# Kernel optimization log

Measured on AMD Instinct MI355X. Metric: run time of the kernel, lower is better.

The kernel has to match this reference:

```python
import jax, jax.numpy as jnp
import numpy as np

T, B, E, H = 64, 64, 128, 256
N_ITEMS, N_DATA = 50000, 20000
EPS = 1e-8


def setup_inputs() -> dict:
    key = jax.random.key(0)
    ks = jax.random.split(key, 20)
    lengths = jnp.sort(jax.random.randint(ks[0], (B,), 1, T + 1))[::-1]
    lengths = lengths.at[0].set(T)  # pack_padded_sequence expects max length first
    x = jax.random.randint(ks[1], (T, B), 1, N_ITEMS)
    tmask = jnp.arange(T)[:, None] < lengths[None, :]
    x = jnp.where(tmask, x, 0)  # padding index 0
    s = 0.05
    emb_table = (jax.random.normal(ks[2], (N_ITEMS, E)) * s).at[0].set(0.0)  # padding_idx=0
    data_embeddings = jax.random.normal(ks[3], (N_DATA, E)) * s
    return {
        'x': x, 'lengths': lengths,
        'emb_table': emb_table, 'data_embeddings': data_embeddings,
        'W_ih': jax.random.normal(ks[4], (4 * H, E)) * s,
        'W_hh': jax.random.normal(ks[5], (4 * H, H)) * s,
        'b_ih': jax.random.normal(ks[6], (4 * H,)) * s,
        'b_hh': jax.random.normal(ks[7], (4 * H,)) * s,
        'Wq': jax.random.normal(ks[8], (H, H)) * s, 'bq': jax.random.normal(ks[9], (H,)) * s,
        'Wk': jax.random.normal(ks[10], (H, H)) * s, 'bk': jax.random.normal(ks[11], (H,)) * s,
        'Wv': jax.random.normal(ks[12], (H, H)) * s, 'bv': jax.random.normal(ks[13], (H,)) * s,
        'W_out': jax.random.normal(ks[14], (E, H)) * s, 'b_out': jax.random.normal(ks[15], (E,)) * s,
    }


def _forward(x, lengths, emb_table, data_embeddings, W_ih, W_hh, b_ih, b_hh,
             Wq, bq, Wk, bk, Wv, bv, W_out, b_out):
    t_len, b_sz = x.shape
    e_dim = emb_table.shape[1]
    h_dim = W_hh.shape[1]

    embs0 = emb_table[x]  # (T, B, E); dropout is identity in eval mode
    initial_embs = jax.lax.stop_gradient(embs0)  # .clone().detach() in original

    # PositionalEncoding: original slices by x.size(1) == batch dim (faithful quirk)
    pos = jnp.arange(b_sz, dtype=jnp.float32)[:, None]
    div = jnp.exp(jnp.arange(0, e_dim, 2, dtype=jnp.float32) * (-jnp.log(10000.0) / e_dim))
    enc = jnp.stack([jnp.sin(pos * div), jnp.cos(pos * div)], axis=-1).reshape(b_sz, e_dim)
    embs = embs0 + enc[None, :, :]  # broadcast over time

    # single-layer LSTM over time (gate order i, f, g, o)
    def step(carry, x_t):
        h, c = carry
        gates = x_t @ W_ih.T + h @ W_hh.T + (b_ih + b_hh)  # (B, 4H)
        i, f, g, o = jnp.split(gates, 4, axis=-1)
        c = jax.nn.sigmoid(f) * c + jax.nn.sigmoid(i) * jnp.tanh(g)
        h = jax.nn.sigmoid(o) * jnp.tanh(c)
        return (h, c), h

    h0 = jnp.zeros((b_sz, h_dim), embs.dtype)
    (_, _), lstm_out = jax.lax.scan(step, (h0, h0), embs)  # (T, B, H)

    # pack/pad round-trip zeroes outputs past each length (LSTM is causal)
    tmask = jnp.arange(t_len)[:, None] < lengths[None, :]  # (T, B)
    lstm_out = lstm_out * tmask[:, :, None]
    lstm_out = lstm_out.transpose(1, 0, 2)  # (B, T, H)

    padding_mask = jnp.sum(lstm_out, axis=-1) != 0  # (B, T)

    q = lstm_out @ Wq.T + bq
    k = lstm_out @ Wk.T + bk
    v = lstm_out @ Wv.T + bv
    score = jnp.einsum('bth,bsh->bts', q, k) / jnp.sqrt(jnp.float32(h_dim))
    score = jnp.where(padding_mask[:, None, :], score, -jnp.inf)
    attn = jax.nn.softmax(score, axis=2)
    weighted = jnp.einsum('bts,bsh->bth', attn, v)  # (B, T, H)
    attn_output = jnp.mean(weighted, axis=1) @ W_out.T + b_out  # (B, E)

    # kNN: fused normalize + matmul + argmin + gather over all T at once
    qn = initial_embs / jnp.clip(jnp.linalg.norm(initial_embs, axis=-1, keepdims=True), EPS)
    dn = data_embeddings / jnp.clip(jnp.linalg.norm(data_embeddings, axis=-1, keepdims=True), EPS)
    sims = jnp.einsum('tbe,ne->tbn', qn, dn)  # (T, B, N_DATA)
    idx = jnp.argmax(sims, axis=-1)  # argmin of (1 - sim)
    closest = jnp.mean(data_embeddings[idx], axis=0)  # (B, E)

    attn_output = attn_output * closest
    return attn_output @ emb_table.T  # (B, n_items)


def reference(x, lengths, emb_table, data_embeddings, W_ih, W_hh, b_ih, b_hh,
              Wq, bq, Wk, bk, Wv, bv, W_out, b_out):
    return _forward(x, lengths, emb_table, data_embeddings, W_ih, W_hh, b_ih, b_hh,
                    Wq, bq, Wk, bk, Wv, bv, W_out, b_out)
```

## Files before the change

kernel.cpp:

```cpp
#include <hip/hip_runtime.h>

typedef unsigned int uint;
typedef unsigned short ushort;
typedef unsigned long long u64;

#define NITEMS 50000
#define NDATA  20000
#define BLKCAP 4096u
#define OVCAP  65536u

#define OFF_LSTMOUT   0x0000000ULL
#define OFF_HX        0x0400000ULL
#define OFF_HXM       0x0440000ULL
#define OFF_PACKED    0x0480000ULL
#define OFF_PACKED2   0x0488000ULL
#define OFF_HITCNTS   0x0490000ULL
#define OFF_OHITCNT   0x0490800ULL
#define MEMSET_BYTES  0x0491000ULL
#define OFF_QMARGIN   0x0491000ULL
#define OFF_XW        0x05A0000ULL
#define OFF_QKV       0x15A0000ULL
#define OFF_HITBUF    OFF_QKV
#define OFF_WIHT      0x21A0000ULL
#define OFF_WQKVT     0x2220000ULL
#define OFF_BIASIH    0x22E0000ULL
#define OFF_BQKV      0x22E1000ULL
#define OFF_DNSCALE   0x22E2000ULL
#define OFF_AV        0x22FE000ULL
#define OFF_DEMB16    0x2306000ULL
#define OFF_A16       0x27E8000ULL
#define OFF_OVF       0x28E8000ULL

__device__ __forceinline__ ushort f2bf(float f) {
  union { float f; uint u; } v; v.f = f;
  uint u = v.u;
  return (ushort)((u + 0x7FFFu + ((u >> 16) & 1u)) >> 16);
}
__device__ __forceinline__ uint fkey(float f) {
  union { float f; uint u; } v; v.f = f;
  return (v.u & 0x80000000u) ? ~v.u : (v.u | 0x80000000u);
}
__device__ __forceinline__ u64 shfl_xor_u64(u64 v, int off) {
  uint lo = (uint)v, hi = (uint)(v >> 32);
  lo = (uint)__shfl_xor((int)lo, off);
  hi = (uint)__shfl_xor((int)hi, off);
  return ((u64)hi << 32) | (u64)lo;
}

typedef __attribute__((ext_vector_type(8))) short short8;
typedef __attribute__((ext_vector_type(4))) float floatx4;

#define R32(M) M(0) M(1) M(2) M(3) M(4) M(5) M(6) M(7) M(8) M(9) M(10) M(11) \
  M(12) M(13) M(14) M(15) M(16) M(17) M(18) M(19) M(20) M(21) M(22) M(23) \
  M(24) M(25) M(26) M(27) M(28) M(29) M(30) M(31)

#define HIX(j) ((j) + (((j) >> 7) << 2))

#define LBAR() do { \
  __builtin_amdgcn_sched_barrier(0); \
  asm volatile("s_waitcnt lgkmcnt(0)" ::: "memory"); \
  __builtin_amdgcn_s_barrier(); \
  __builtin_amdgcn_sched_barrier(0); \
} while (0)

__global__ __launch_bounds__(256) void prep_kernel(
    const int* __restrict__ x,
    const float* __restrict__ emb, const float* __restrict__ demb,
    const float* __restrict__ W_ih,
    const float* __restrict__ Wq, const float* __restrict__ Wk, const float* __restrict__ Wv,
    const float* __restrict__ b_ih, const float* __restrict__ b_hh,
    const float* __restrict__ bq, const float* __restrict__ bk, const float* __restrict__ bv,
    float* __restrict__ dnscale, ushort* __restrict__ demb16, ushort* __restrict__ a16,
    float* __restrict__ wiht, float* __restrict__ wqkvt,
    float* __restrict__ biasih, float* __restrict__ bqkv,
    float* __restrict__ qmargin, u64* __restrict__ packed2)
{
  int blk = blockIdx.x, tid = threadIdx.x;
  if (blk < 5000) {
    int row = blk * 4 + (tid >> 6);
    int lane = tid & 63;
    float2 d = *(const float2*)(demb + (size_t)row * 128 + lane * 2);
    float s = d.x * d.x + d.y * d.y;
    for (int off = 32; off; off >>= 1) s += __shfl_xor(s, off);
    if (lane == 0) dnscale[row] = 1.0f / fmaxf(sqrtf(s), 1e-8f);
  } else if (blk < 6250) {
    size_t base = ((size_t)(blk - 5000) * 256 + tid) * 8;
    float4 f1 = *(const float4*)(demb + base);
    float4 f2 = *(const float4*)(demb + base + 4);
    uint4 o;
    o.x = (uint)f2bf(f1.x) | ((uint)f2bf(f1.y) << 16);
    o.y = (uint)f2bf(f1.z) | ((uint)f2bf(f1.w) << 16);
    o.z = (uint)f2bf(f2.x) | ((uint)f2bf(f2.y) << 16);
    o.w = (uint)f2bf(f2.z) | ((uint)f2bf(f2.w) << 16);
    *(uint4*)(demb16 + base) = o;
  } else if (blk < 6506) {
    int idx = (blk - 6250) * 256 + tid;
    int m = idx >> 4, seg = idx & 15;
    const float* src = emb + (size_t)x[m] * 128 + seg * 8;
    float4 f1 = *(const float4*)(src);
    float4 f2 = *(const float4*)(src + 4);
    uint4 o;
    o.x = (uint)f2bf(f1.x) | ((uint)f2bf(f1.y) << 16);
    o.y = (uint)f2bf(f1.z) | ((uint)f2bf(f1.w) << 16);
    o.z = (uint)f2bf(f2.x) | ((uint)f2bf(f2.y) << 16);
    o.w = (uint)f2bf(f2.z) | ((uint)f2bf(f2.w) << 16);
    *(uint4*)(a16 + (size_t)m * 128 + seg * 8) = o;
  } else if (blk < 7018) {
    int f = (blk - 6506) * 256 + tid;
    int r = f >> 7, e = f & 127;
    wiht[e * 1024 + r] = W_ih[f];
  } else if (blk < 7786) {
    int f = (blk - 7018) * 256 + tid;
    int w = f >> 16; int rem = f & 65535;
    int r = rem >> 8, e = rem & 255;
    const float* src = (w == 0) ? Wq : (w == 1) ? Wk : Wv;
    wqkvt[e * 768 + w * 256 + r] = src[rem];
  } else if (blk < 7790) {
    int idx = (blk - 7786) * 256 + tid;
    if (idx < 1024) biasih[idx] = b_ih[idx] + b_hh[idx];
  } else if (blk < 7793) {
    int idx = (blk - 7790) * 256 + tid;
    if (idx < 768) {
      int w = idx >> 8; int r = idx & 255;
      const float* src = (w == 0) ? bq : (w == 1) ? bk : bv;
      bqkv[idx] = src[r];
    }
  } else {
    int row = (blk - 7793) * 4 + (tid >> 6);
    int lane = tid & 63;
    float2 d = *(const float2*)(emb + (size_t)x[row] * 128 + lane * 2);
    float s = d.x * d.x + d.y * d.y;
    for (int off = 32; off; off >>= 1) s += __shfl_xor(s, off);
    if (lane == 0) {
      if (s == 0.f) {
        qmargin[row] = -1e30f;
        packed2[row] = ((u64)fkey(0.0f) << 32) | 0xFFFFFFFFull;
      } else {
        qmargin[row] = 0.017f * sqrtf(s) + 1e-5f;
      }
    }
  }
}

__global__ __launch_bounds__(256) void xw_kernel(
    const int* __restrict__ x, const float* __restrict__ emb,
    const float* __restrict__ wiht, const float* __restrict__ biasih,
    float* __restrict__ xW)
{
  __shared__ __align__(16) float At[128 * 16];
  int blk = blockIdx.x, tid = threadIdx.x;
  int m0 = blk * 16;
  for (int c = 0; c < 8; ++c) {
    int idx = c * 256 + tid;
    int mm = idx >> 7, e = idx & 127;
    int m = m0 + mm;
    int bcol = m & 63;
    int xv = x[m];
    float val = emb[(size_t)xv * 128 + e];
    int j = e >> 1;
    float arg = (float)bcol * __expf((float)j * -0.14391157f);
    val += (e & 1) ? cosf(arg) : sinf(arg);
    At[e * 16 + mm] = val;
  }
  __syncthreads();
  int quad = tid >> 6, l = tid & 63;
  for (int rp = 0; rp < 4; ++rp) {
    int r = rp * 256 + l * 4;
    float acc[4][4] = {};
    for (int e = 0; e < 128; ++e) {
      float4 wv4 = *(const float4*)(wiht + e * 1024 + r);
      float4 av4 = *(const float4*)(At + e * 16 + quad * 4);
      float am[4] = {av4.x, av4.y, av4.z, av4.w};
      float wr4[4] = {wv4.x, wv4.y, wv4.z, wv4.w};
      #pragma unroll
      for (int mi = 0; mi < 4; ++mi)
        #pragma unroll
        for (int ri = 0; ri < 4; ++ri)
          acc[mi][ri] += am[mi] * wr4[ri];
    }
    float4 bv4 = *(const float4*)(biasih + r);
    #pragma unroll
    for (int mi = 0; mi < 4; ++mi) {
      size_t m = (size_t)(m0 + quad * 4 + mi);
      float4 o;
      o.x = acc[mi][0] + bv4.x; o.y = acc[mi][1] + bv4.y;
      o.z = acc[mi][2] + bv4.z; o.w = acc[mi][3] + bv4.w;
      *(float4*)(xW + m * 1024 + r) = o;
    }
  }
}

__global__ __launch_bounds__(512, 2) void lstm_knn_kernel(
    const int* __restrict__ lengths, const float* __restrict__ Whh,
    const float* __restrict__ xW, float* __restrict__ lstm_out,
    u64* __restrict__ hx, u64* __restrict__ hxm,
    const ushort* __restrict__ a16, const ushort* __restrict__ demb16,
    const float* __restrict__ dnscale, const float* __restrict__ qmargin,
    u64* __restrict__ packed, uint* __restrict__ hitcnts, uint* __restrict__ ohitcnt,
    uint* __restrict__ hitbuf, uint* __restrict__ ovbuf,
    const int* __restrict__ x, const float* __restrict__ emb,
    const float* __restrict__ demb, u64* __restrict__ packed2)
{
  __shared__ __align__(16) float h_sh[264];
  __shared__ float part_sh[256];
  __shared__ __align__(16) ushort b_sh[2][64 * 144];
  __shared__ uint lcnt;
  int tid = threadIdx.x;

  if (blockIdx.x < 256) {
    int blk = blockIdx.x;
    int b = blk & 63, q = blk >> 6;
    int row_local = tid >> 1, half = tid & 1;
    int gate = row_local >> 6, jloc = row_local & 63;
    int grow = gate * 256 + q * 64 + jloc;
    const float4* wp4 = (const float4*)(Whh + (size_t)grow * 256 + half * 128);
#define WDECL(i) float4 tt##i = wp4[i]; \
  float w##i##x = tt##i.x, w##i##y = tt##i.y, w##i##z = tt##i.z, w##i##w = tt##i.w;
    R32(WDECL)
#define WPIN(i) asm volatile("" : "+v"(w##i##x), "+v"(w##i##y), "+v"(w##i##z), "+v"(w##i##w));
    R32(WPIN)
    int len = lengths[b];
    if (tid < 256) h_sh[HIX(tid)] = 0.f;
    float cval = 0.f;
    int prm = tid - 320;
    int jr = (prm < q * 64) ? prm : prm + 64;
    bool fast_ok = true;
    int j1 = q * 64 + (tid - 64);
    float xw0 = 0.f, xw1 = 0.f, xw2 = 0.f, xw3 = 0.f;
    if (tid < 64) {
      const float* xwrow = xW + ((size_t)0 * 64 + b) * 1024 + q * 64 + tid;
      xw0 = xwrow[0]; xw1 = xwrow[256]; xw2 = xwrow[512]; xw3 = xwrow[768];
    }
    __syncthreads();
    for (int t = 0; t < len; ++t) {
      float nx0 = 0.f, nx1 = 0.f, nx2 = 0.f, nx3 = 0.f;
      if (tid < 64 && t + 1 < len) {
        const float* xwrow = xW + ((size_t)(t + 1) * 64 + b) * 1024 + q * 64 + tid;
        nx0 = xwrow[0]; nx1 = xwrow[256]; nx2 = xwrow[512]; nx3 = xwrow[768];
      }
      float hprev = 0.f;
      if (tid >= 64 && tid < 128 && t > 0) hprev = h_sh[HIX(j1)];
      const float4* h4 = (const float4*)(h_sh + half * 132);
      float a[4] = {0.f, 0.f, 0.f, 0.f};
#define WACC(i) { float4 hv_ = h4[i]; \
    a[(i) & 3] += w##i##x * hv_.x + w##i##y * hv_.y + w##i##z * hv_.z + w##i##w * hv_.w; }
      R32(WACC)
      float acc = (a[0] + a[2]) + (a[1] + a[3]);
      acc += __shfl_xor(acc, 1);
      if (!half) part_sh[row_local] = acc;
      LBAR();
      if (tid < 64) {
        float gi = part_sh[tid]       + xw0;
        float gf = part_sh[64 + tid]  + xw1;
        float gg = part_sh[128 + tid] + xw2;
        float go = part_sh[192 + tid] + xw3;
        float ii = 1.f / (1.f + __expf(-gi));
        float ff = 1.f / (1.f + __expf(-gf));
        float oo = 1.f / (1.f + __expf(-go));
        float tg = 1.f - 2.f / (1.f + __expf(2.f * gg));
        cval = ff * cval + ii * tg;
        float tc = 1.f - 2.f / (1.f + __expf(2.f * cval));
        float hv = oo * tc;
        int j = q * 64 + tid;
        union { float f; uint u; } cu; cu.f = hv;
        u64 pk = ((u64)cu.u << 32) | (u64)(uint)(t + 1);
        size_t slot = ((size_t)((t + 1) & 1) * 64 + b) * 256 + j;
        __builtin_amdgcn_sched_barrier(0);
        asm volatile("s_waitcnt vmcnt(4)" ::: "memory");
        asm volatile("global_store_dwordx2 %0, %1, off"
                     :: "v"(hxm + slot), "v"(pk) : "memory");
        __hip_atomic_store(hx + slot, pk, __ATOMIC_RELAXED, __HIP_MEMORY_SCOPE_AGENT);
        h_sh[HIX(j)] = hv;
        xw0 = nx0; xw1 = nx1; xw2 = nx2; xw3 = nx3;
      } else if (tid < 128) {
        if (t > 0) lstm_out[((size_t)b * 64 + (t - 1)) * 256 + j1] = hprev;
      } else if (tid >= 320 && t + 1 < len) {
        size_t slot = ((size_t)((t + 1) & 1) * 64 + b) * 256 + jr;
        uint want = (uint)(t + 1);
        u64 v = 0;
        bool got = false;
        if (fast_ok) {
          const u64* ms = hxm + slot;
          for (int tries = 0; tries < 32; ++tries) {
            asm volatile("global_load_dwordx2 %0, %1, off sc0\n\t"
                         "s_waitcnt vmcnt(0)"
                         : "=&v"(v) : "v"(ms) : "memory");
            if ((uint)v == want) { got = true; break; }
          }
          if (!got && t > 0) fast_ok = false;
        }
        if (!got) {
          const u64* as = hx + slot;
          int guard = 0;
          while (true) {
            v = __hip_atomic_load(as, __ATOMIC_RELAXED, __HIP_MEMORY_SCOPE_AGENT);
            if ((uint)v == want || ++guard > (1 << 24)) break;
          }
        }
        union { uint u; float f; } cv; cv.u = (uint)(v >> 32);
        h_sh[HIX(jr)] = cv.f;
      }
      LBAR();
    }
    if (tid >= 64 && tid < 128) {
      float hl = h_sh[HIX(j1)];
      lstm_out[((size_t)b * 64 + (len - 1)) * 256 + j1] = hl;
    }
    return;
  }

  int nb = blockIdx.x - 256;
  int mt = nb >> 3;
  int cpair = nb & 7;
  int w8 = tid >> 6;
  int s = w8 >> 2, wv2 = w8 & 3;
  int lane = tid & 63;
  int col = lane & 15, quad = lane >> 4;
  int M0 = mt * 128;
  short8 afrag[4];
  {
    int mrow = M0 + s * 64 + wv2 * 16 + col;
    #pragma unroll
    for (int kf = 0; kf < 4; ++kf)
      afrag[kf] = *(const short8*)(a16 + (size_t)mrow * 128 + kf * 32 + quad * 8);
  }
  float qm[4];
  #pragma unroll
  for (int r = 0; r < 4; ++r)
    qm[r] = qmargin[M0 + s * 64 + wv2 * 16 + quad * 4 + r];
  int srow = tid >> 4, sseg = tid & 15;
  const int niter = 20;

  for (int c2 = 0; c2 < 2; ++c2) {
    int chunk = cpair * 2 + c2;
    int kb = mt * 16 + chunk;
    int nbase = chunk * 1250, nend = nbase + 1250;
    if (tid == 0) lcnt = 0;
    float best[4] = {-1e30f, -1e30f, -1e30f, -1e30f};
    int bidx[4] = {};
    uint4 stg[2]; float scr[4];

    #pragma unroll
    for (int p = 0; p < 2; ++p) {
      int n = nbase + p * 32 + srow;
      uint4 v = {0u,0u,0u,0u};
      if (n < nend) v = *(const uint4*)(demb16 + (size_t)n * 128 + sseg * 8);
      stg[p] = v;
    }
    #pragma unroll
    for (int ns = 0; ns < 4; ++ns) {
      int n = nbase + ns * 16 + col;
      scr[ns] = (n < nend) ? dnscale[n] : 0.f;
    }
    for (int it = 0; it < niter; ++it) {
      int n0 = nbase + it * 64;
      ushort* bsh = b_sh[it & 1];
      #pragma unroll
      for (int p = 0; p < 2; ++p)
        *(uint4*)(&bsh[(p * 32 + srow) * 144 + sseg * 8]) = stg[p];
      float mysc[4] = {scr[0], scr[1], scr[2], scr[3]};
      __syncthreads();
      if (it + 1 < niter) {
        int nbn = n0 + 64;
        #pragma unroll
        for (int p = 0; p < 2; ++p) {
          int n = nbn + p * 32 + srow;
          uint4 v = {0u,0u,0u,0u};
          if (n < nend) v = *(const uint4*)(demb16 + (size_t)n * 128 + sseg * 8);
          stg[p] = v;
        }
        #pragma unroll
        for (int ns = 0; ns < 4; ++ns) {
          int n = nbn + ns * 16 + col;
          scr[ns] = (n < nend) ? dnscale[n] : 0.f;
        }
      }
      #pragma unroll
      for (int ns = 0; ns < 4; ++ns) {
        short8 bfr[4];
        #pragma unroll
        for (int kf = 0; kf < 4; ++kf)
          bfr[kf] = *(const short8*)(&bsh[(ns * 16 + col) * 144 + kf * 32 + quad * 8]);
        int n = n0 + ns * 16 + col;
        float sc = mysc[ns];
        bool valid = (n < nend);
        floatx4 acc = {0.f, 0.f, 0.f, 0.f};
        #pragma unroll
        for (int kf = 0; kf < 4; ++kf)
          acc = __builtin_amdgcn_mfma_f32_16x16x32_bf16(afrag[kf], bfr[kf], acc, 0, 0, 0);
        #pragma unroll
        for (int r = 0; r < 4; ++r) {
          float sim = acc[r] * sc;
          if (valid && sim > best[r]) { best[r] = sim; bidx[r] = n; }
        }
      }
    }
    float thr[4];
    #pragma unroll
    for (int r = 0; r < 4; ++r) {
      u64 p = ((u64)fkey(best[r]) << 32) | (u64)(0xFFFFFFFFu - (uint)bidx[r]);
      #pragma unroll
      for (int off = 1; off < 16; off <<= 1) {
        u64 o = shfl_xor_u64(p, off);
        if (o > p) p = o;
      }
      int m = M0 + s * 64 + wv2 * 16 + quad * 4 + r;
      union { uint u; float f; } bu;
      uint k = (uint)(p >> 32);
      bu.u = (k & 0x80000000u) ? (k & 0x7FFFFFFFu) : ~k;
      thr[r] = bu.f - qm[r];
      if (col == 0)
        atomicMax((unsigned long long*)&packed[m], (unsigned long long)p);
    }
    __syncthreads();

    uint* myregion = hitbuf + (size_t)kb * BLKCAP;
    uint* ovregion = ovbuf;
    #pragma unroll
    for (int p = 0; p < 2; ++p) {
      int n = nbase + p * 32 + srow;
      uint4 v = {0u,0u,0u,0u};
      if (n < nend) v = *(const uint4*)(demb16 + (size_t)n * 128 + sseg * 8);
      stg[p] = v;
    }
    #pragma unroll
    for (int ns = 0; ns < 4; ++ns) {
      int n = nbase + ns * 16 + col;
      scr[ns] = (n < nend) ? dnscale[n] : 0.f;
    }
    for (int it = 0; it < niter; ++it) {
      int n0 = nbase + it * 64;
      ushort* bsh = b_sh[it & 1];
      #pragma unroll
      for (int p = 0; p < 2; ++p)
        *(uint4*)(&bsh[(p * 32 + srow) * 144 + sseg * 8]) = stg[p];
      float mysc[4] = {scr[0], scr[1], scr[2], scr[3]};
      __syncthreads();
      if (it + 1 < niter) {
        int nbn = n0 + 64;
        #pragma unroll
        for (int p = 0; p < 2; ++p) {
          int n = nbn + p * 32 + srow;
          uint4 v = {0u,0u,0u,0u};
          if (n < nend) v = *(const uint4*)(demb16 + (size_t)n * 128 + sseg * 8);
          stg[p] = v;
        }
        #pragma unroll
        for (int ns = 0; ns < 4; ++ns) {
          int n = nbn + ns * 16 + col;
          scr[ns] = (n < nend) ? dnscale[n] : 0.f;
        }
      }
      #pragma unroll
      for (int ns = 0; ns < 4; ++ns) {
        short8 bfr[4];
        #pragma unroll
        for (int kf = 0; kf < 4; ++kf)
          bfr[kf] = *(const short8*)(&bsh[(ns * 16 + col) * 144 + kf * 32 + quad * 8]);
        int n = n0 + ns * 16 + col;
        float sc = mysc[ns];
        bool valid = (n < nend);
        floatx4 acc = {0.f, 0.f, 0.f, 0.f};
        #pragma unroll
        for (int kf = 0; kf < 4; ++kf)
          acc = __builtin_amdgcn_mfma_f32_16x16x32_bf16(afrag[kf], bfr[kf], acc, 0, 0, 0);
        #pragma unroll
        for (int r = 0; r < 4; ++r) {
          float sim = acc[r] * sc;
          bool hit = valid && (sim >= thr[r]);
          u64 mask = __ballot(hit);
          if (mask) {
            uint lcntv = (uint)__popcll(mask);
            int leader = __ffsll((unsigned long long)mask) - 1;
            uint base = 0;
            if (lane == leader) base = atomicAdd(&lcnt, lcntv);
            base = (uint)__shfl((int)base, leader);
            if (hit) {
              uint pos = base + (uint)__popcll(mask & ((1ull << lane) - 1ull));
              uint mm = (uint)(M0 + s * 64 + wv2 * 16 + quad * 4 + r);
              uint rec = (mm << 15) | (uint)n;
              if (pos < BLKCAP) {
                myregion[pos] = rec;
              } else {
                uint op = atomicAdd(ohitcnt, 1u);
                if (op < OVCAP) ovregion[op] = rec;
              }
            }
          }
        }
      }
    }
    __syncthreads();
    if (tid == 0) hitcnts[kb] = lcnt;
    uint rcnt = lcnt; if (rcnt > BLKCAP) rcnt = BLKCAP;
    for (uint h = tid; h < rcnt; h += 512) {
      uint rec = myregion[h];
      uint m = rec >> 15, n = rec & 0x7FFFu;
      if (m >= 4096 || n >= NDATA) continue;
      const float* qr = emb + (size_t)x[m] * 128;
      const float* dr = demb + (size_t)n * 128;
      double p = 0.0;
      #pragma unroll 8
      for (int e = 0; e < 128; e += 2) {
        float2 qv = *(const float2*)(qr + e);
        float2 dv = *(const float2*)(dr + e);
        p += (double)qv.x * (double)dv.x + (double)qv.y * (double)dv.y;
      }
      float sx = (float)(p * (double)dnscale[n]);
      u64 key = ((u64)fkey(sx) << 32) | (u64)(0xFFFFFFFFu - n);
      atomicMax((unsigned long long*)&packed2[m], (unsigned long long)key);
    }
    __syncthreads();
  }
}

__global__ __launch_bounds__(256) void fused_post_kernel(
    const float* __restrict__ lstm_out, const float* __restrict__ wqkvt,
    const float* __restrict__ bqkv, float* __restrict__ qkv,
    const u64* __restrict__ packed, const uint* __restrict__ ohitcnt,
    const uint* __restrict__ ovbuf, const int* __restrict__ x,
    const float* __restrict__ emb, const float* __restrict__ demb,
    const float* __restrict__ dnscale, u64* __restrict__ packed2)
{
  __shared__ __align__(16) float At[256 * 16];
  int blk = blockIdx.x, tid = threadIdx.x;
  if (blk < 256) {
    int m0 = blk * 16;
    for (int c = 0; c < 16; ++c)
      At[tid * 16 + c] = lstm_out[((size_t)m0 + c) * 256 + tid];
    __syncthreads();
    int quad = tid >> 6, l = tid & 63;
    for (int rp = 0; rp < 3; ++rp) {
      int r = rp * 256 + l * 4;
      float acc[4][4] = {};
      for (int e = 0; e < 256; ++e) {
        float4 wv4 = *(const float4*)(wqkvt + (size_t)e * 768 + r);
        float4 av4 = *(const float4*)(At + e * 16 + quad * 4);
        float am[4] = {av4.x, av4.y, av4.z, av4.w};
        float wr4[4] = {wv4.x, wv4.y, wv4.z, wv4.w};
        #pragma unroll
        for (int mi = 0; mi < 4; ++mi)
          #pragma unroll
          for (int ri = 0; ri < 4; ++ri)
            acc[mi][ri] += am[mi] * wr4[ri];
      }
      float4 bv4 = *(const float4*)(bqkv + r);
      #pragma unroll
      for (int mi = 0; mi < 4; ++mi) {
        size_t m = (size_t)(m0 + quad * 4 + mi);
        float4 o;
        o.x = acc[mi][0] + bv4.x; o.y = acc[mi][1] + bv4.y;
        o.z = acc[mi][2] + bv4.z; o.w = acc[mi][3] + bv4.w;
        *(float4*)(qkv + m * 768 + r) = o;
      }
    }
    return;
  }
  if (blk < 272) {
    uint m = (uint)(blk - 256) * 256 + tid;
    uint n = 0xFFFFFFFFu - (uint)(packed[m] & 0xFFFFFFFFull);
    if (n < NDATA) {
      const float* qr = emb + (size_t)x[m] * 128;
      const float* dr = demb + (size_t)n * 128;
      double p = 0.0;
      #pragma unroll 8
      for (int e = 0; e < 128; e += 2) {
        float2 qv = *(const float2*)(qr + e);
        float2 dv = *(const float2*)(dr + e);
        p += (double)qv.x * (double)dv.x + (double)qv.y * (double)dv.y;
      }
      float sx = (float)(p * (double)dnscale[n]);
      u64 key = ((u64)fkey(sx) << 32) | (u64)(0xFFFFFFFFu - n);
      atomicMax((unsigned long long*)&packed2[m], (unsigned long long)key);
    }
    return;
  }
  uint cnt = *ohitcnt; if (cnt > OVCAP) cnt = OVCAP;
  for (uint h = (uint)(blk - 272) * 256 + tid; h < cnt; h += 16 * 256) {
    uint rec = ovbuf[h];
    uint m = rec >> 15, n = rec & 0x7FFFu;
    if (m >= 4096 || n >= NDATA) continue;
    const float* qr = emb + (size_t)x[m] * 128;
    const float* dr = demb + (size_t)n * 128;
    double p = 0.0;
    #pragma unroll 8
    for (int e = 0; e < 128; e += 2) {
      float2 qv = *(const float2*)(qr + e);
      float2 dv = *(const float2*)(dr + e);
      p += (double)qv.x * (double)dv.x + (double)qv.y * (double)dv.y;
    }
    float sx = (float)(p * (double)dnscale[n]);
    u64 key = ((u64)fkey(sx) << 32) | (u64)(0xFFFFFFFFu - n);
    atomicMax((unsigned long long*)&packed2[m], (unsigned long long)key);
  }
}

__global__ __launch_bounds__(256) void attn_kernel(
    const float* __restrict__ qkv, const int* __restrict__ lengths,
    const u64* __restrict__ packed2, const float* __restrict__ demb,
    const float* __restrict__ W_out, const float* __restrict__ b_out,
    float* __restrict__ av)
{
  __shared__ float k_sh[64 * 257];
  __shared__ __align__(16) float q_sh[4 * 256];
  __shared__ float wpart[4 * 64];
  __shared__ float wtot[64];
  __shared__ float out_sh[256];
  int b = blockIdx.x, tid = threadIdx.x;
  int wv = tid >> 6, lane = tid & 63;
  int len = lengths[b];
  for (int s = 0; s < 64; ++s)
    k_sh[s * 257 + tid] = qkv[((size_t)b * 64 + s) * 768 + 256 + tid];
  float clv = 0.f;
  if (tid < 128) {
    float sum = 0.f;
    for (int t = 0; t < 64; ++t) {
      uint low = (uint)(packed2[t * 64 + b] & 0xFFFFFFFFull);
      uint n = 0xFFFFFFFFu - low;
      if (n >= NDATA) n = 0;
      sum += demb[(size_t)n * 128 + tid];
    }
    clv = sum * (1.0f / 64.0f);
  }
  wpart[tid] = 0.f;
  for (int tq = 0; tq < 16; ++tq) {
    __syncthreads();
    #pragma unroll
    for (int c = 0; c < 4; ++c)
      q_sh[c * 256 + tid] = qkv[((size_t)b * 64 + tq * 4 + c) * 768 + tid];
    __syncthreads();
    const float* krow = k_sh + lane * 257;
    const float* qrow = q_sh + wv * 256;
    float sc = 0.f;
    #pragma unroll 8
    for (int h = 0; h < 256; ++h)
      sc += qrow[h] * krow[h];
    sc *= 0.0625f;
    bool vs = (lane < len);
    float scm = vs ? sc : -1e30f;
    float mx = scm;
    for (int off = 32; off; off >>= 1) mx = fmaxf(mx, __shfl_xor(mx, off));
    float e = vs ? __expf(sc - mx) : 0.f;
    float sum = e;
    for (int off = 32; off; off >>= 1) sum += __shfl_xor(sum, off);
    wpart[wv * 64 + lane] += e / sum;
  }
  __syncthreads();
  if (tid < 64)
    wtot[tid] = (wpart[tid] + wpart[64 + tid] + wpart[128 + tid] + wpart[192 + tid]) * (1.0f / 64.0f);
  __syncthreads();
  {
    float acc = 0.f;
    for (int s = 0; s < 64; ++s)
      acc += wtot[s] * qkv[((size_t)b * 64 + s) * 768 + 512 + tid];
    out_sh[tid] = acc;
  }
  __syncthreads();
  if (tid < 128) {
    const float4* wr = (const float4*)(W_out + (size_t)tid * 256);
    float p = b_out[tid];
    #pragma unroll
    for (int c = 0; c < 64; ++c) {
      float4 u = wr[c];
      p += out_sh[c * 4 + 0] * u.x + out_sh[c * 4 + 1] * u.y
         + out_sh[c * 4 + 2] * u.z + out_sh[c * 4 + 3] * u.w;
    }
    av[tid * 64 + b] = p * clv;
  }
}

__global__ __launch_bounds__(256) void final_kernel(
    const float* __restrict__ emb, const float* __restrict__ av,
    float* __restrict__ out)
{
  int i = blockIdx.x * 256 + threadIdx.x;
  if (i >= NITEMS) return;
  const float4* row = (const float4*)(emb + (size_t)i * 128);
  float acc[64];
  #pragma unroll
  for (int bb = 0; bb < 64; ++bb) acc[bb] = 0.f;
  for (int e4 = 0; e4 < 32; ++e4) {
    float4 u = row[e4];
    float wvv[4] = {u.x, u.y, u.z, u.w};
    const float* ab = av + e4 * 4 * 64;
    #pragma unroll
    for (int j = 0; j < 4; ++j) {
      #pragma unroll
      for (int bb = 0; bb < 64; ++bb)
        acc[bb] += wvv[j] * ab[j * 64 + bb];
    }
  }
  #pragma unroll
  for (int bb = 0; bb < 64; ++bb)
    out[(size_t)bb * NITEMS + i] = acc[bb];
}

extern "C" void kernel_launch(void* const* d_in, const int* in_sizes, int n_in,
                              void* d_out, int out_size, void* d_ws, size_t ws_size,
                              hipStream_t stream)
{
  const int*   x       = (const int*)d_in[0];
  const int*   lengths = (const int*)d_in[1];
  const float* emb     = (const float*)d_in[2];
  const float* demb    = (const float*)d_in[3];
  const float* W_ih    = (const float*)d_in[4];
  const float* W_hh    = (const float*)d_in[5];
  const float* b_ih    = (const float*)d_in[6];
  const float* b_hh    = (const float*)d_in[7];
  const float* Wq      = (const float*)d_in[8];
  const float* bq      = (const float*)d_in[9];
  const float* Wk      = (const float*)d_in[10];
  const float* bk      = (const float*)d_in[11];
  const float* Wv      = (const float*)d_in[12];
  const float* bv      = (const float*)d_in[13];
  const float* W_out   = (const float*)d_in[14];
  const float* b_out   = (const float*)d_in[15];

  char* ws = (char*)d_ws;
  float*  lstm_out = (float*)(ws + OFF_LSTMOUT);
  u64*    hx       = (u64*)(ws + OFF_HX);
  u64*    hxm      = (u64*)(ws + OFF_HXM);
  u64*    packed   = (u64*)(ws + OFF_PACKED);
  u64*    packed2  = (u64*)(ws + OFF_PACKED2);
  uint*   hitcnts  = (uint*)(ws + OFF_HITCNTS);
  uint*   ohitcnt  = (uint*)(ws + OFF_OHITCNT);
  float*  qmargin  = (float*)(ws + OFF_QMARGIN);
  uint*   hitbuf   = (uint*)(ws + OFF_HITBUF);
  uint*   ovbuf    = (uint*)(ws + OFF_OVF);
  float*  xW       = (float*)(ws + OFF_XW);
  float*  qkv      = (float*)(ws + OFF_QKV);
  float*  wiht     = (float*)(ws + OFF_WIHT);
  float*  wqkvt    = (float*)(ws + OFF_WQKVT);
  float*  biasih   = (float*)(ws + OFF_BIASIH);
  float*  bqkv     = (float*)(ws + OFF_BQKV);
  float*  dnscale  = (float*)(ws + OFF_DNSCALE);
  float*  av       = (float*)(ws + OFF_AV);
  ushort* demb16   = (ushort*)(ws + OFF_DEMB16);
  ushort* a16      = (ushort*)(ws + OFF_A16);

  hipMemsetAsync(d_ws, 0, (size_t)MEMSET_BYTES, stream);

  hipLaunchKernelGGL(prep_kernel, dim3(8817), dim3(256), 0, stream,
                     x, emb, demb, W_ih, Wq, Wk, Wv, b_ih, b_hh, bq, bk, bv,
                     dnscale, demb16, a16, wiht, wqkvt, biasih, bqkv,
                     qmargin, packed2);
  hipLaunchKernelGGL(xw_kernel, dim3(256), dim3(256), 0, stream,
                     x, emb, wiht, biasih, xW);
  hipLaunchKernelGGL(lstm_knn_kernel, dim3(512), dim3(512), 0, stream,
                     lengths, W_hh, xW, lstm_out, hx, hxm,
                     a16, demb16, dnscale, qmargin, packed, hitcnts, ohitcnt,
                     hitbuf, ovbuf, x, emb, demb, packed2);
  hipLaunchKernelGGL(fused_post_kernel, dim3(288), dim3(256), 0, stream,
                     lstm_out, wqkvt, bqkv, qkv, packed, ohitcnt, ovbuf,
                     x, emb, demb, dnscale, packed2);
  hipLaunchKernelGGL(attn_kernel, dim3(64), dim3(256), 0, stream,
                     qkv, lengths, packed2, demb, W_out, b_out, av);
  hipLaunchKernelGGL(final_kernel, dim3(196), dim3(256), 0, stream,
                     emb, av, (float*)d_out);
}
```

Before: 584.1 us.

## Load kNN B fragments directly from global memory instead of LDS staging

Removes the double-buffered shared-memory staging of data embeddings in both kNN passes. Each lane now loads its bf16 B fragments straight from global memory (mostly L2-resident) and feeds them to MFMA. The per-iteration __syncthreads barriers go away, and the LDS footprint shrinks, which could raise occupancy. The cost is that the explicit prefetch overlap is lost and global load latency is exposed on every MFMA group.

```diff
diff --git a/kernel.cpp b/kernel.cpp
--- a/kernel.cpp
+++ b/kernel.cpp
@@ -203,7 +203,6 @@
 {
   __shared__ __align__(16) float h_sh[264];
   __shared__ float part_sh[256];
-  __shared__ __align__(16) ushort b_sh[2][64 * 144];
   __shared__ uint lcnt;
   int tid = threadIdx.x;
 
@@ -328,7 +327,6 @@
   #pragma unroll
   for (int r = 0; r < 4; ++r)
     qm[r] = qmargin[M0 + s * 64 + wv2 * 16 + quad * 4 + r];
-  int srow = tid >> 4, sseg = tid & 15;
   const int niter = 20;
 
   for (int c2 = 0; c2 < 2; ++c2) {
@@ -336,58 +334,24 @@
     int kb = mt * 16 + chunk;
     int nbase = chunk * 1250, nend = nbase + 1250;
     if (tid == 0) lcnt = 0;
+    __syncthreads();
     float best[4] = {-1e30f, -1e30f, -1e30f, -1e30f};
     int bidx[4] = {};
-    uint4 stg[2]; float scr[4];
-
-    #pragma unroll
-    for (int p = 0; p < 2; ++p) {
-      int n = nbase + p * 32 + srow;
-      uint4 v = {0u,0u,0u,0u};
-      if (n < nend) v = *(const uint4*)(demb16 + (size_t)n * 128 + sseg * 8);
-      stg[p] = v;
-    }
-    #pragma unroll
-    for (int ns = 0; ns < 4; ++ns) {
-      int n = nbase + ns * 16 + col;
-      scr[ns] = (n < nend) ? dnscale[n] : 0.f;
-    }
+
     for (int it = 0; it < niter; ++it) {
       int n0 = nbase + it * 64;
-      ushort* bsh = b_sh[it & 1];
-      #pragma unroll
-      for (int p = 0; p < 2; ++p)
-        *(uint4*)(&bsh[(p * 32 + srow) * 144 + sseg * 8]) = stg[p];
-      float mysc[4] = {scr[0], scr[1], scr[2], scr[3]};
-      __syncthreads();
-      if (it + 1 < niter) {
-        int nbn = n0 + 64;
-        #pragma unroll
-        for (int p = 0; p < 2; ++p) {
-          int n = nbn + p * 32 + srow;
-          uint4 v = {0u,0u,0u,0u};
-          if (n < nend) v = *(const uint4*)(demb16 + (size_t)n * 128 + sseg * 8);
-          stg[p] = v;
-        }
-        #pragma unroll
-        for (int ns = 0; ns < 4; ++ns) {
-          int n = nbn + ns * 16 + col;
-          scr[ns] = (n < nend) ? dnscale[n] : 0.f;
-        }
-      }
       #pragma unroll
       for (int ns = 0; ns < 4; ++ns) {
-        short8 bfr[4];
-        #pragma unroll
-        for (int kf = 0; kf < 4; ++kf)
-          bfr[kf] = *(const short8*)(&bsh[(ns * 16 + col) * 144 + kf * 32 + quad * 8]);
         int n = n0 + ns * 16 + col;
-        float sc = mysc[ns];
         bool valid = (n < nend);
+        int nc = valid ? n : (NDATA - 1);
+        const ushort* bp = demb16 + (size_t)nc * 128 + quad * 8;
+        float sc = valid ? dnscale[n] : 0.f;
         floatx4 acc = {0.f, 0.f, 0.f, 0.f};
-        #pragma unroll
-        for (int kf = 0; kf < 4; ++kf)
-          acc = __builtin_amdgcn_mfma_f32_16x16x32_bf16(afrag[kf], bfr[kf], acc, 0, 0, 0);
+        acc = __builtin_amdgcn_mfma_f32_16x16x32_bf16(afrag[0], *(const short8*)(bp),      acc, 0, 0, 0);
+        acc = __builtin_amdgcn_mfma_f32_16x16x32_bf16(afrag[1], *(const short8*)(bp + 32), acc, 0, 0, 0);
+        acc = __builtin_amdgcn_mfma_f32_16x16x32_bf16(afrag[2], *(const short8*)(bp + 64), acc, 0, 0, 0);
+        acc = __builtin_amdgcn_mfma_f32_16x16x32_bf16(afrag[3], *(const short8*)(bp + 96), acc, 0, 0, 0);
         #pragma unroll
         for (int r = 0; r < 4; ++r) {
           float sim = acc[r] * sc;
@@ -412,58 +376,23 @@
       if (col == 0)
         atomicMax((unsigned long long*)&packed[m], (unsigned long long)p);
     }
-    __syncthreads();
 
     uint* myregion = hitbuf + (size_t)kb * BLKCAP;
     uint* ovregion = ovbuf;
-    #pragma unroll
-    for (int p = 0; p < 2; ++p) {
-      int n = nbase + p * 32 + srow;
-      uint4 v = {0u,0u,0u,0u};
-      if (n < nend) v = *(const uint4*)(demb16 + (size_t)n * 128 + sseg * 8);
-      stg[p] = v;
-    }
-    #pragma unroll
-    for (int ns = 0; ns < 4; ++ns) {
-      int n = nbase + ns * 16 + col;
-      scr[ns] = (n < nend) ? dnscale[n] : 0.f;
-    }
     for (int it = 0; it < niter; ++it) {
       int n0 = nbase + it * 64;
-      ushort* bsh = b_sh[it & 1];
-      #pragma unroll
-      for (int p = 0; p < 2; ++p)
-        *(uint4*)(&bsh[(p * 32 + srow) * 144 + sseg * 8]) = stg[p];
-      float mysc[4] = {scr[0], scr[1], scr[2], scr[3]};
-      __syncthreads();
-      if (it + 1 < niter) {
-        int nbn = n0 + 64;
-        #pragma unroll
-        for (int p = 0; p < 2; ++p) {
-          int n = nbn + p * 32 + srow;
-          uint4 v = {0u,0u,0u,0u};
-          if (n < nend) v = *(const uint4*)(demb16 + (size_t)n * 128 + sseg * 8);
-          stg[p] = v;
-        }
-        #pragma unroll
-        for (int ns = 0; ns < 4; ++ns) {
-          int n = nbn + ns * 16 + col;
-          scr[ns] = (n < nend) ? dnscale[n] : 0.f;
-        }
-      }
       #pragma unroll
       for (int ns = 0; ns < 4; ++ns) {
-        short8 bfr[4];
-        #pragma unroll
-        for (int kf = 0; kf < 4; ++kf)
-          bfr[kf] = *(const short8*)(&bsh[(ns * 16 + col) * 144 + kf * 32 + quad * 8]);
         int n = n0 + ns * 16 + col;
-        float sc = mysc[ns];
         bool valid = (n < nend);
+        int nc = valid ? n : (NDATA - 1);
+        const ushort* bp = demb16 + (size_t)nc * 128 + quad * 8;
+        float sc = valid ? dnscale[n] : 0.f;
         floatx4 acc = {0.f, 0.f, 0.f, 0.f};
-        #pragma unroll
-        for (int kf = 0; kf < 4; ++kf)
-          acc = __builtin_amdgcn_mfma_f32_16x16x32_bf16(afrag[kf], bfr[kf], acc, 0, 0, 0);
+        acc = __builtin_amdgcn_mfma_f32_16x16x32_bf16(afrag[0], *(const short8*)(bp),      acc, 0, 0, 0);
+        acc = __builtin_amdgcn_mfma_f32_16x16x32_bf16(afrag[1], *(const short8*)(bp + 32), acc, 0, 0, 0);
+        acc = __builtin_amdgcn_mfma_f32_16x16x32_bf16(afrag[2], *(const short8*)(bp + 64), acc, 0, 0, 0);
+        acc = __builtin_amdgcn_mfma_f32_16x16x32_bf16(afrag[3], *(const short8*)(bp + 96), acc, 0, 0, 0);
         #pragma unroll
         for (int r = 0; r < 4; ++r) {
           float sim = acc[r] * sc;
```

New measurement: 760.6 us. +30.2%, slower.
